# Kernel optimization log

Hardware: AMD Instinct MI355X
Metric: run time of the kernel (lower is better)

Reference implementation:

```python
import jax, jax.numpy as jnp
import numpy as np

B, NS, NQ = 128, 128, 512
D_IN, D_OUT = 256, 64


def setup_inputs() -> dict:
    key = jax.random.key(0)
    ks = jax.random.split(key, 6)
    return {
        "phi_support": jax.random.normal(ks[0], (B, NS, D_IN), dtype=jnp.float32),
        "y_support": jax.random.normal(ks[1], (B, NS, D_OUT), dtype=jnp.float32),
        "phi_query": jax.random.normal(ks[2], (B, NQ, D_IN), dtype=jnp.float32),
        "y_query": jax.random.normal(ks[3], (B, NQ, D_OUT), dtype=jnp.float32),
        # xavier-uniform-ish params
        "m_prior": jax.random.uniform(ks[4], (D_IN, D_OUT), minval=-1.0, maxval=1.0) * np.sqrt(6.0 / (D_IN + D_OUT)),
        "S_inv_prior_asym": jax.random.uniform(ks[5], (D_IN, D_IN), minval=-1.0, maxval=1.0) * np.sqrt(6.0 / (2 * D_IN)),
        "sig_eps": jnp.array([0.1], dtype=jnp.float32),
    }


def reference(phi_support, y_support, phi_query, y_query, m_prior, S_inv_prior_asym, sig_eps):
    alpha = 1.0
    d_out = m_prior.shape[1]
    # prior precision (symmetric PSD by construction) and natural-param prior mean
    S_inv_prior = alpha * (S_inv_prior_asym @ S_inv_prior_asym.T)          # [D_in, D_in]
    m_prior_nat = S_inv_prior @ m_prior                                     # [D_in, D_out]
    # posterior precision / covariance per task (nobs > 0 branch)
    S_inv = jnp.einsum('bni,bnj->bij', phi_support, phi_support) + S_inv_prior  # [B, D_in, D_in]
    S = jnp.linalg.inv(S_inv)                                               # batched small inverse
    rhs = jnp.einsum('bni,bnk->bik', phi_support, y_support) + m_prior_nat  # [B, D_in, D_out]
    m = S @ rhs                                                             # [B, D_in, D_out]
    # predictive mean and spread
    mu = phi_query @ m                                                      # [B, Q, D_out]
    spread_fac = 1.0 + jnp.einsum('bqi,bij,bqj->bq', phi_query, S, phi_query)  # [B, Q]
    # sig = spread_fac (x) (eye * sig_eps) : diagonal [B, Q, D_out, D_out]
    diag = jnp.eye(d_out, dtype=mu.dtype) * sig_eps                         # [D_out, D_out]
    sig = spread_fac[..., None, None] * diag
    # nll: logdet of diagonal sig + quadratic form with its inverse (diag -> reciprocal)
    logdet = d_out * (jnp.log(spread_fac) + jnp.log(sig_eps))               # [B, Q]
    resid = y_query - mu
    quadf = jnp.sum(resid * resid, axis=-1) / (spread_fac * sig_eps)        # [B, Q]
    nll = logdet.mean() + quadf.mean()
    return mu, sig, nll
```

## Files before the change

kernel.cpp:

```cpp
#include <hip/hip_runtime.h>
#include <math.h>

#define B_T   128
#define NS    128
#define NQ    512
#define DIN   256
#define DOUT  64

#define MU_SIZE  (B_T*NQ*DOUT)
#define SIG_SIZE (B_T*NQ*DOUT*DOUT)
#define NLL_IDX  (MU_SIZE + SIG_SIZE)

__global__ __launch_bounds__(256) void k_prior_sp(const float* __restrict__ A,
                                                  double* __restrict__ Sp,
                                                  double* __restrict__ NLLACC) {
    __shared__ float Ai[16][260];
    __shared__ float Aj[16][260];
    int bi = blockIdx.x;
    int i0 = (bi >> 4) << 4;
    int j0 = (bi & 15) << 4;
    int tid = threadIdx.x;
    if (bi == 0 && tid == 0) NLLACC[0] = 0.0;
    for (int idx = tid; idx < 16 * 256; idx += 256) {
        int r = idx >> 8, c = idx & 255;
        Ai[r][c] = A[(i0 + r) * 256 + c];
        Aj[r][c] = A[(j0 + r) * 256 + c];
    }
    __syncthreads();
    int r = tid >> 4, c = tid & 15;
    double acc = 0.0;
    for (int k = 0; k < 256; ++k)
        acc += (double)Ai[r][k] * (double)Aj[c][k];
    Sp[(i0 + r) * 256 + (j0 + c)] = acc;
}

__global__ __launch_bounds__(64) void k_prior_mpn(const double* __restrict__ Sp,
                                                  const float* __restrict__ MP,
                                                  double* __restrict__ MPN) {
    int i = blockIdx.x, k = threadIdx.x;
    double acc = 0.0;
    for (int t = 0; t < 256; ++t)
        acc += Sp[i * 256 + t] * (double)MP[t * 64 + k];
    MPN[i * 64 + k] = acc;
}

__global__ __launch_bounds__(256) void k_build_G(const float* __restrict__ PHI,
                                                 const double* __restrict__ Sp,
                                                 double* __restrict__ G) {
    __shared__ float As[128][64];
    __shared__ float Bs[128][64];
    int b = blockIdx.x;
    int by = blockIdx.y;
    int ti = 0;
    while (((ti + 1) * (ti + 2)) / 2 <= by) ti++;
    int tj = by - (ti * (ti + 1)) / 2;
    int i0 = ti * 64, j0 = tj * 64;
    int tid = threadIdx.x;
    const float* Pb = PHI + b * (NS * DIN);
    for (int idx = tid; idx < 128 * 64; idx += 256) {
        int n = idx >> 6, c = idx & 63;
        As[n][c] = Pb[n * 256 + i0 + c];
        Bs[n][c] = Pb[n * 256 + j0 + c];
    }
    __syncthreads();
    int tx = tid & 15, ty = tid >> 4;
    double acc[4][4];
#pragma unroll
    for (int r = 0; r < 4; ++r)
#pragma unroll
        for (int s = 0; s < 4; ++s) acc[r][s] = 0.0;
    for (int n = 0; n < 128; ++n) {
        float a0 = As[n][4 * ty + 0], a1 = As[n][4 * ty + 1];
        float a2 = As[n][4 * ty + 2], a3 = As[n][4 * ty + 3];
        float b0 = Bs[n][4 * tx + 0], b1 = Bs[n][4 * tx + 1];
        float b2 = Bs[n][4 * tx + 2], b3 = Bs[n][4 * tx + 3];
        acc[0][0] += (double)a0 * b0; acc[0][1] += (double)a0 * b1;
        acc[0][2] += (double)a0 * b2; acc[0][3] += (double)a0 * b3;
        acc[1][0] += (double)a1 * b0; acc[1][1] += (double)a1 * b1;
        acc[1][2] += (double)a1 * b2; acc[1][3] += (double)a1 * b3;
        acc[2][0] += (double)a2 * b0; acc[2][1] += (double)a2 * b1;
        acc[2][2] += (double)a2 * b2; acc[2][3] += (double)a2 * b3;
        acc[3][0] += (double)a3 * b0; acc[3][1] += (double)a3 * b1;
        acc[3][2] += (double)a3 * b2; acc[3][3] += (double)a3 * b3;
    }
    double* Gb = G + b * 65536;
#pragma unroll
    for (int r = 0; r < 4; ++r) {
        int i = i0 + 4 * ty + r;
#pragma unroll
        for (int s = 0; s < 4; ++s) {
            int j = j0 + 4 * tx + s;
            Gb[i * 256 + j] = acc[r][s] + Sp[i * 256 + j];
        }
    }
}

__global__ __launch_bounds__(256) void k_build_rhs(const float* __restrict__ PHI,
                                                   const float* __restrict__ Y,
                                                   const double* __restrict__ MPN,
                                                   double* __restrict__ RHS) {
    __shared__ float As[128][64];
    __shared__ float Ys[128][64];
    int b = blockIdx.x, i0 = blockIdx.y * 64, tid = threadIdx.x;
    const float* Pb = PHI + b * (NS * DIN);
    const float* Yb = Y + b * (NS * DOUT);
    for (int idx = tid; idx < 128 * 64; idx += 256) {
        int n = idx >> 6, c = idx & 63;
        As[n][c] = Pb[n * 256 + i0 + c];
        Ys[n][c] = Yb[n * 64 + c];
    }
    __syncthreads();
    int tx = tid & 15, ty = tid >> 4;
    double acc[4][4];
#pragma unroll
    for (int r = 0; r < 4; ++r)
#pragma unroll
        for (int s = 0; s < 4; ++s) acc[r][s] = 0.0;
    for (int n = 0; n < 128; ++n) {
        float a0 = As[n][4 * ty + 0], a1 = As[n][4 * ty + 1];
        float a2 = As[n][4 * ty + 2], a3 = As[n][4 * ty + 3];
        float y0 = Ys[n][4 * tx + 0], y1 = Ys[n][4 * tx + 1];
        float y2 = Ys[n][4 * tx + 2], y3 = Ys[n][4 * tx + 3];
        acc[0][0] += (double)a0 * y0; acc[0][1] += (double)a0 * y1;
        acc[0][2] += (double)a0 * y2; acc[0][3] += (double)a0 * y3;
        acc[1][0] += (double)a1 * y0; acc[1][1] += (double)a1 * y1;
        acc[1][2] += (double)a1 * y2; acc[1][3] += (double)a1 * y3;
        acc[2][0] += (double)a2 * y0; acc[2][1] += (double)a2 * y1;
        acc[2][2] += (double)a2 * y2; acc[2][3] += (double)a2 * y3;
        acc[3][0] += (double)a3 * y0; acc[3][1] += (double)a3 * y1;
        acc[3][2] += (double)a3 * y2; acc[3][3] += (double)a3 * y3;
    }
    double* Rb = RHS + b * 16384;
#pragma unroll
    for (int r = 0; r < 4; ++r) {
        int i = i0 + 4 * ty + r;
#pragma unroll
        for (int s = 0; s < 4; ++s) {
            int kc = 4 * tx + s;
            Rb[i * 64 + kc] = acc[r][s] + MPN[i * 64 + kc];
        }
    }
}

__global__ __launch_bounds__(256) void k_cholinv(double* __restrict__ G,
                                                 double* __restrict__ LT,
                                                 double* __restrict__ TI,
                                                 float* __restrict__ TIF) {
    __shared__ double S[8192];
    int b = blockIdx.x, tid = threadIdx.x;
    double* Gb = G + b * 65536;
    double* LTb = LT + b * 65536;
    double* TIb = TI + b * 65536;
    float* TIFb = TIF + b * 65536;

    double* P = S;
#define PCH(p, r) P[(p) * 258 + (r)]
    for (int k0 = 0; k0 < 256; k0 += 16) {
        int rows = 256 - k0;
        for (int idx = tid; idx < rows * 16; idx += 256) {
            int r = k0 + (idx >> 4), p = idx & 15;
            PCH(p, r) = Gb[r * 256 + k0 + p];
        }
        __syncthreads();
        for (int p = 0; p < 16; ++p) {
            int k = k0 + p;
            if (tid >= k) {
                double v = PCH(p, tid);
                for (int p2 = 0; p2 < p; ++p2) v -= PCH(p2, tid) * PCH(p2, k);
                PCH(p, tid) = v;
            }
            __syncthreads();
            double d = sqrt(fmax(PCH(p, k), 1e-300));
            double inv = 1.0 / d;
            if (tid > k) PCH(p, tid) *= inv;
            else if (tid == k) PCH(p, tid) = d;
            __syncthreads();
        }
        for (int p = 0; p < 16; ++p) {
            int k = k0 + p;
            if (tid >= k) LTb[k * 256 + tid] = PCH(p, tid);
        }
        int ty = tid >> 4, tx = tid & 15;
        for (int i2 = k0 + 16 + 2 * ty; i2 < 256; i2 += 32) {
            double pa[16], pb[16];
#pragma unroll
            for (int p = 0; p < 16; ++p) { pa[p] = PCH(p, i2); pb[p] = PCH(p, i2 + 1); }
            for (int j2 = k0 + 16 + 2 * tx; j2 <= i2 + 1; j2 += 32) {
                double g00 = 0.0, g01 = 0.0, g10 = 0.0, g11 = 0.0;
#pragma unroll
                for (int p = 0; p < 16; ++p) {
                    double q0 = PCH(p, j2), q1 = PCH(p, j2 + 1);
                    g00 += pa[p] * q0; g01 += pa[p] * q1;
                    g10 += pb[p] * q0; g11 += pb[p] * q1;
                }
                if (j2 <= i2)     Gb[i2 * 256 + j2]           -= g00;
                if (j2 + 1 <= i2) Gb[i2 * 256 + j2 + 1]       -= g01;
                Gb[(i2 + 1) * 256 + j2] -= g10;
                if (j2 <= i2)     Gb[(i2 + 1) * 256 + j2 + 1] -= g11;
            }
        }
        __syncthreads();
    }
#undef PCH

    double* SHD = S;
    for (int idx = tid; idx < 65536; idx += 256) {
        int i = idx >> 8, k = idx & 255;
        if (k > i) { TIb[idx] = 0.0; TIFb[idx] = 0.0f; }
    }
    for (int idx = tid; idx < 8192; idx += 256) {
        int g = idx >> 10, rem = idx & 1023, k = rem >> 5, i = rem & 31;
        SHD[idx] = LTb[(32 * g + k) * 256 + 32 * g + i];
    }
    __syncthreads();
    {
        int g = tid >> 5, j = tid & 31;
        const double* D = SHD + g * 1024;
        double x[32];
#pragma unroll
        for (int i = 0; i < 32; ++i) {
            double s = (i == j) ? 1.0 : 0.0;
#pragma unroll
            for (int k = 0; k < i; ++k) {
                double lv = D[k * 32 + i];
                s -= (k >= j) ? lv * x[k] : 0.0;
            }
            double inv = 1.0 / D[i * 32 + i];
            x[i] = (i >= j) ? s * inv : 0.0;
        }
#pragma unroll
        for (int i = 0; i < 32; ++i) {
            int gi = 32 * g + i, gj = 32 * g + j;
            TIb[gi * 256 + gj] = x[i];
            TIFb[gi * 256 + gj] = (float)x[i];
        }
    }
    __syncthreads();
    double* Bsh = SHD;
    int j = tid & 31, ig = tid >> 5;
    for (int I = 1; I < 8; ++I) {
        for (int J = I - 1; J >= 0; --J) {
            double acc[4] = {0.0, 0.0, 0.0, 0.0};
            for (int K = J; K < I; ++K) {
                for (int kk = 0; kk < 32; ++kk) {
                    double tv = TIb[(32 * K + kk) * 256 + 32 * J + j];
#pragma unroll
                    for (int r = 0; r < 4; ++r) {
                        double lv = LTb[(32 * K + kk) * 256 + 32 * I + ig * 4 + r];
                        acc[r] += lv * tv;
                    }
                }
            }
            __syncthreads();
#pragma unroll
            for (int r = 0; r < 4; ++r) Bsh[(ig * 4 + r) * 32 + j] = acc[r];
            __syncthreads();
            double c[4] = {0.0, 0.0, 0.0, 0.0};
            for (int k = 0; k < 32; ++k) {
                double bv = Bsh[k * 32 + j];
#pragma unroll
                for (int r = 0; r < 4; ++r) {
                    double dv = TIb[(32 * I + ig * 4 + r) * 256 + 32 * I + k];
                    c[r] -= dv * bv;
                }
            }
#pragma unroll
            for (int r = 0; r < 4; ++r) {
                int gi = 32 * I + ig * 4 + r, gj = 32 * J + j;
                TIb[gi * 256 + gj] = c[r];
                TIFb[gi * 256 + gj] = (float)c[r];
            }
        }
        __syncthreads();
    }
}

__global__ __launch_bounds__(256) void k_gemm_Z(const double* __restrict__ TI,
                                                const double* __restrict__ RHS,
                                                double* __restrict__ Z) {
    __shared__ double As[32][64];
    __shared__ double Bs[64][64];
    int b = blockIdx.x, i0 = blockIdx.y * 32;
    int tid = threadIdx.x, c = tid & 63, rg = tid >> 6;
    const double* TIb = TI + b * 65536;
    const double* Rb = RHS + b * 16384;
    double* Zb = Z + b * 16384;
    double acc[8] = {};
    for (int k0 = 0; k0 <= i0; k0 += 64) {
        for (int idx = tid; idx < 2048; idx += 256) {
            int r = idx >> 6, kk = idx & 63;
            As[r][kk] = TIb[(i0 + r) * 256 + k0 + kk];
        }
        for (int idx = tid; idx < 4096; idx += 256) {
            int kk = idx >> 6, cc = idx & 63;
            Bs[kk][cc] = Rb[(k0 + kk) * 64 + cc];
        }
        __syncthreads();
        for (int kk = 0; kk < 64; ++kk) {
            double bv = Bs[kk][c];
#pragma unroll
            for (int r = 0; r < 8; ++r)
                acc[r] += As[rg * 8 + r][kk] * bv;
        }
        __syncthreads();
    }
#pragma unroll
    for (int r = 0; r < 8; ++r)
        Zb[(i0 + rg * 8 + r) * 64 + c] = acc[r];
}

__global__ __launch_bounds__(256) void k_gemm_M(const double* __restrict__ TI,
                                                const double* __restrict__ Z,
                                                double* __restrict__ M) {
    __shared__ double As[64][32];
    __shared__ double Bs[64][64];
    int b = blockIdx.x, i0 = blockIdx.y * 32;
    int tid = threadIdx.x, c = tid & 63, rg = tid >> 6;
    const double* TIb = TI + b * 65536;
    const double* Zb = Z + b * 16384;
    double* Mb = M + b * 16384;
    double acc[8] = {};
    for (int k0 = (i0 >> 6) << 6; k0 < 256; k0 += 64) {
        for (int idx = tid; idx < 2048; idx += 256) {
            int kk = idx >> 5, ri = idx & 31;
            As[kk][ri] = TIb[(k0 + kk) * 256 + i0 + ri];
        }
        for (int idx = tid; idx < 4096; idx += 256) {
            int kk = idx >> 6, cc = idx & 63;
            Bs[kk][cc] = Zb[(k0 + kk) * 64 + cc];
        }
        __syncthreads();
        for (int kk = 0; kk < 64; ++kk) {
            double bv = Bs[kk][c];
#pragma unroll
            for (int r = 0; r < 8; ++r)
                acc[r] += As[kk][rg * 8 + r] * bv;
        }
        __syncthreads();
    }
#pragma unroll
    for (int r = 0; r < 8; ++r)
        Mb[(i0 + rg * 8 + r) * 64 + c] = acc[r];
}

__global__ __launch_bounds__(256) void k_spread_gemm(const float* __restrict__ PHIQ,
                                                     const float* __restrict__ TIF,
                                                     float* __restrict__ PSUM) {
    __shared__ float Qs[64][65];
    __shared__ float Ts[64][65];
    int b = blockIdx.x, q0 = blockIdx.y * 64, I = blockIdx.z, i0 = I * 64;
    int tid = threadIdx.x, tx = tid & 15, ty = tid >> 4;
    const float* Qb = PHIQ + b * (NQ * DIN) + q0 * DIN;
    const float* Tb = TIF + b * 65536;
    float acc[4][4];
#pragma unroll
    for (int r = 0; r < 4; ++r)
#pragma unroll
        for (int s = 0; s < 4; ++s) acc[r][s] = 0.0f;
    for (int k0 = 0; k0 <= i0; k0 += 64) {
        for (int idx = tid; idx < 4096; idx += 256) {
            int r = idx >> 6, c = idx & 63;
            Qs[r][c] = Qb[r * 256 + k0 + c];
            Ts[c][r] = Tb[(i0 + r) * 256 + k0 + c];
        }
        __syncthreads();
        for (int kk = 0; kk < 64; ++kk) {
            float a0 = Qs[4 * ty + 0][kk], a1 = Qs[4 * ty + 1][kk];
            float a2 = Qs[4 * ty + 2][kk], a3 = Qs[4 * ty + 3][kk];
            float b0 = Ts[kk][4 * tx + 0], b1 = Ts[kk][4 * tx + 1];
            float b2 = Ts[kk][4 * tx + 2], b3 = Ts[kk][4 * tx + 3];
            acc[0][0] += a0 * b0; acc[0][1] += a0 * b1; acc[0][2] += a0 * b2; acc[0][3] += a0 * b3;
            acc[1][0] += a1 * b0; acc[1][1] += a1 * b1; acc[1][2] += a1 * b2; acc[1][3] += a1 * b3;
            acc[2][0] += a2 * b0; acc[2][1] += a2 * b1; acc[2][2] += a2 * b2; acc[2][3] += a2 * b3;
            acc[3][0] += a3 * b0; acc[3][1] += a3 * b1; acc[3][2] += a3 * b2; acc[3][3] += a3 * b3;
        }
        __syncthreads();
    }
#pragma unroll
    for (int r = 0; r < 4; ++r) {
        float p = acc[r][0] * acc[r][0] + acc[r][1] * acc[r][1]
                + acc[r][2] * acc[r][2] + acc[r][3] * acc[r][3];
        p += __shfl_down(p, 8, 16);
        p += __shfl_down(p, 4, 16);
        p += __shfl_down(p, 2, 16);
        p += __shfl_down(p, 1, 16);
        if (tx == 0) PSUM[(size_t)(b * 4 + I) * 512 + q0 + 4 * ty + r] = p;
    }
}

__global__ __launch_bounds__(256) void k_mu_nll(const float* __restrict__ PHIQ,
                                                const double* __restrict__ M,
                                                const float* __restrict__ YQ,
                                                const float* __restrict__ PSUM,
                                                const float* __restrict__ SE,
                                                float* __restrict__ SPREAD,
                                                double* __restrict__ NLLACC,
                                                float* __restrict__ MU) {
    __shared__ float Qs[64][65];
    __shared__ float Ms[64][64];
    __shared__ double nred[64];
    int b = blockIdx.x, q0 = blockIdx.y * 64, tid = threadIdx.x;
    int tx = tid & 15, ty = tid >> 4;
    const float* Qb = PHIQ + b * (NQ * DIN) + q0 * DIN;
    const double* Mb = M + b * 16384;
    float acc[4][4];
#pragma unroll
    for (int r = 0; r < 4; ++r)
#pragma unroll
        for (int s = 0; s < 4; ++s) acc[r][s] = 0.0f;
    for (int c0 = 0; c0 < 256; c0 += 64) {
        for (int idx = tid; idx < 4096; idx += 256) {
            int r = idx >> 6, c = idx & 63;
            Qs[r][c] = Qb[r * 256 + c0 + c];
            Ms[r][c] = (float)Mb[(c0 + r) * 64 + c];
        }
        __syncthreads();
        for (int kk = 0; kk < 64; ++kk) {
            float a0 = Qs[4 * ty + 0][kk], a1 = Qs[4 * ty + 1][kk];
            float a2 = Qs[4 * ty + 2][kk], a3 = Qs[4 * ty + 3][kk];
            float b0 = Ms[kk][4 * tx + 0], b1 = Ms[kk][4 * tx + 1];
            float b2 = Ms[kk][4 * tx + 2], b3 = Ms[kk][4 * tx + 3];
            acc[0][0] += a0 * b0; acc[0][1] += a0 * b1; acc[0][2] += a0 * b2; acc[0][3] += a0 * b3;
            acc[1][0] += a1 * b0; acc[1][1] += a1 * b1; acc[1][2] += a1 * b2; acc[1][3] += a1 * b3;
            acc[2][0] += a2 * b0; acc[2][1] += a2 * b1; acc[2][2] += a2 * b2; acc[2][3] += a2 * b3;
            acc[3][0] += a3 * b0; acc[3][1] += a3 * b1; acc[3][2] += a3 * b2; acc[3][3] += a3 * b3;
        }
        __syncthreads();
    }
    float se = SE[0];
#pragma unroll
    for (int r = 0; r < 4; ++r) {
        int q = q0 + 4 * ty + r;
        float4 v = make_float4(acc[r][0], acc[r][1], acc[r][2], acc[r][3]);
        *(float4*)&MU[(b * NQ + q) * 64 + 4 * tx] = v;
        float4 y = *(const float4*)&YQ[(size_t)(b * NQ + q) * 64 + 4 * tx];
        float dx = y.x - v.x, dy = y.y - v.y, dz = y.z - v.z, dw = y.w - v.w;
        float qs = dx * dx + dy * dy + dz * dz + dw * dw;
        qs += __shfl_down(qs, 8, 16);
        qs += __shfl_down(qs, 4, 16);
        qs += __shfl_down(qs, 2, 16);
        qs += __shfl_down(qs, 1, 16);
        if (tx == 0) {
            float sp = 1.0f + PSUM[(size_t)(b * 4 + 0) * 512 + q]
                            + PSUM[(size_t)(b * 4 + 1) * 512 + q]
                            + PSUM[(size_t)(b * 4 + 2) * 512 + q]
                            + PSUM[(size_t)(b * 4 + 3) * 512 + q];
            SPREAD[b * 512 + q] = sp;
            float val = 64.0f * (logf(sp) + logf(se)) + qs / (sp * se);
            nred[ty * 4 + r] = (double)val;
        }
    }
    __syncthreads();
    for (int s = 32; s > 0; s >>= 1) {
        if (tid < s) nred[tid] += nred[tid + s];
        __syncthreads();
    }
    if (tid == 0) atomicAdd(NLLACC, nred[0] * (1.0 / 65536.0));
}

__global__ void k_nll_final(const double* __restrict__ NLLACC,
                            float* __restrict__ out) {
    if (threadIdx.x == 0) out[NLL_IDX] = (float)NLLACC[0];
}

__global__ __launch_bounds__(256) void k_sig(const float* __restrict__ SPREAD,
                                             const float* __restrict__ SE,
                                             float* __restrict__ out) {
    __shared__ float sv_s;
    int bq = blockIdx.x, tid = threadIdx.x;
    if (tid == 0) sv_s = SPREAD[bq] * SE[0];
    __syncthreads();
    float sv = sv_s;
    float* base = out + (size_t)MU_SIZE + (size_t)bq * 4096;
    int i = tid >> 2;
    int jb = (tid & 3) << 4;
    int d = i - jb;
    float vals[16];
#pragma unroll
    for (int t = 0; t < 16; ++t) vals[t] = (t == d) ? sv : 0.0f;
    float4* p = (float4*)(base + tid * 16);
    p[0] = make_float4(vals[0], vals[1], vals[2], vals[3]);
    p[1] = make_float4(vals[4], vals[5], vals[6], vals[7]);
    p[2] = make_float4(vals[8], vals[9], vals[10], vals[11]);
    p[3] = make_float4(vals[12], vals[13], vals[14], vals[15]);
}

extern "C" void kernel_launch(void* const* d_in, const int* in_sizes, int n_in,
                              void* d_out, int out_size, void* d_ws, size_t ws_size,
                              hipStream_t stream) {
    const float* PHI_S = (const float*)d_in[0];
    const float* Y_S   = (const float*)d_in[1];
    const float* PHI_Q = (const float*)d_in[2];
    const float* Y_Q   = (const float*)d_in[3];
    const float* MP    = (const float*)d_in[4];
    const float* AP    = (const float*)d_in[5];
    const float* SE    = (const float*)d_in[6];
    float* out = (float*)d_out;

    double* scratch = (double*)(out + MU_SIZE);
    double* G    = scratch;
    double* LT   = G + 8388608;
    double* RHS  = LT + 8388608;
    double* Z    = RHS + 2097152;
    double* TI   = Z + 2097152;
    double* Spd  = TI + 8388608;
    double* MPN  = Spd + 65536;
    float*  TIF  = (float*)(MPN + 16384);
    float*  PSUM = TIF + 8388608;
    float*  SPREAD = (float*)d_ws;
    double* NLLACC = (double*)((char*)d_ws + 65536 * 4);

    k_prior_sp   <<<256, 256, 0, stream>>>(AP, Spd, NLLACC);
    k_prior_mpn  <<<256, 64, 0, stream>>>(Spd, MP, MPN);
    k_build_G    <<<dim3(B_T, 10), 256, 0, stream>>>(PHI_S, Spd, G);
    k_build_rhs  <<<dim3(B_T, 4), 256, 0, stream>>>(PHI_S, Y_S, MPN, RHS);
    k_cholinv    <<<B_T, 256, 0, stream>>>(G, LT, TI, TIF);
    k_gemm_Z     <<<dim3(B_T, 8), 256, 0, stream>>>(TI, RHS, Z);
    k_gemm_M     <<<dim3(B_T, 8), 256, 0, stream>>>(TI, Z, RHS);
    k_spread_gemm<<<dim3(B_T, 8, 4), 256, 0, stream>>>(PHI_Q, TIF, PSUM);
    k_mu_nll     <<<dim3(B_T, 8), 256, 0, stream>>>(PHI_Q, RHS, Y_Q, PSUM, SE,
                                                    SPREAD, NLLACC, out);
    k_nll_final  <<<1, 64, 0, stream>>>(NLLACC, out);
    k_sig        <<<65536, 256, 0, stream>>>(SPREAD, SE, out);
}
```

Baseline: 2.244 ms.

## Fuse build, solve and predict kernels; widen Cholesky panels to 32 with 512 threads

Merges the prior-mean, G and RHS construction into one launch, and merges the spread GEMM and the mu/NLL computation into one predict kernel that keeps the spread partials in registers. The Cholesky inverse now uses 32-wide panels with a rotated shared layout, shuffle-based panel factorization and 512 threads, and stages the block inverse updates through shared memory. The two M GEMMs are merged into a single solve kernel, and NLL finalization moves into k_sig. This cuts launches and global round-trips, at the cost of more register pressure and more serial work inside the 32-lane panel factorization.

```diff
diff --git a/kernel.cpp b/kernel.cpp
--- a/kernel.cpp
+++ b/kernel.cpp
@@ -34,164 +34,173 @@
     Sp[(i0 + r) * 256 + (j0 + c)] = acc;
 }
 
-__global__ __launch_bounds__(64) void k_prior_mpn(const double* __restrict__ Sp,
-                                                  const float* __restrict__ MP,
-                                                  double* __restrict__ MPN) {
-    int i = blockIdx.x, k = threadIdx.x;
-    double acc = 0.0;
-    for (int t = 0; t < 256; ++t)
-        acc += Sp[i * 256 + t] * (double)MP[t * 64 + k];
-    MPN[i * 64 + k] = acc;
-}
-
-__global__ __launch_bounds__(256) void k_build_G(const float* __restrict__ PHI,
-                                                 const double* __restrict__ Sp,
-                                                 double* __restrict__ G) {
+__global__ __launch_bounds__(256) void k_build(const float* __restrict__ PHI,
+                                               const float* __restrict__ Y,
+                                               const float* __restrict__ MP,
+                                               const double* __restrict__ Sp,
+                                               double* __restrict__ G,
+                                               double* __restrict__ RHS,
+                                               double* __restrict__ MPNo) {
+    int b = blockIdx.x, by = blockIdx.y, tid = threadIdx.x;
+    if (by == 14) {
+        if (b >= 4) return;
+        for (int out = tid; out < 4096; out += 256) {
+            int r = 64 * b + (out >> 6), cc = out & 63;
+            double acc = 0.0;
+            for (int t = 0; t < 256; ++t)
+                acc += Sp[r * 256 + t] * (double)MP[t * 64 + cc];
+            MPNo[r * 64 + cc] = acc;
+        }
+        return;
+    }
     __shared__ float As[128][64];
     __shared__ float Bs[128][64];
-    int b = blockIdx.x;
-    int by = blockIdx.y;
-    int ti = 0;
-    while (((ti + 1) * (ti + 2)) / 2 <= by) ti++;
-    int tj = by - (ti * (ti + 1)) / 2;
-    int i0 = ti * 64, j0 = tj * 64;
-    int tid = threadIdx.x;
+    int tx = tid & 15, ty = tid >> 4;
     const float* Pb = PHI + b * (NS * DIN);
-    for (int idx = tid; idx < 128 * 64; idx += 256) {
-        int n = idx >> 6, c = idx & 63;
-        As[n][c] = Pb[n * 256 + i0 + c];
-        Bs[n][c] = Pb[n * 256 + j0 + c];
-    }
-    __syncthreads();
-    int tx = tid & 15, ty = tid >> 4;
     double acc[4][4];
 #pragma unroll
     for (int r = 0; r < 4; ++r)
 #pragma unroll
         for (int s = 0; s < 4; ++s) acc[r][s] = 0.0;
-    for (int n = 0; n < 128; ++n) {
-        float a0 = As[n][4 * ty + 0], a1 = As[n][4 * ty + 1];
-        float a2 = As[n][4 * ty + 2], a3 = As[n][4 * ty + 3];
-        float b0 = Bs[n][4 * tx + 0], b1 = Bs[n][4 * tx + 1];
-        float b2 = Bs[n][4 * tx + 2], b3 = Bs[n][4 * tx + 3];
-        acc[0][0] += (double)a0 * b0; acc[0][1] += (double)a0 * b1;
-        acc[0][2] += (double)a0 * b2; acc[0][3] += (double)a0 * b3;
-        acc[1][0] += (double)a1 * b0; acc[1][1] += (double)a1 * b1;
-        acc[1][2] += (double)a1 * b2; acc[1][3] += (double)a1 * b3;
-        acc[2][0] += (double)a2 * b0; acc[2][1] += (double)a2 * b1;
-        acc[2][2] += (double)a2 * b2; acc[2][3] += (double)a2 * b3;
-        acc[3][0] += (double)a3 * b0; acc[3][1] += (double)a3 * b1;
-        acc[3][2] += (double)a3 * b2; acc[3][3] += (double)a3 * b3;
-    }
-    double* Gb = G + b * 65536;
-#pragma unroll
-    for (int r = 0; r < 4; ++r) {
-        int i = i0 + 4 * ty + r;
-#pragma unroll
-        for (int s = 0; s < 4; ++s) {
-            int j = j0 + 4 * tx + s;
-            Gb[i * 256 + j] = acc[r][s] + Sp[i * 256 + j];
-        }
-    }
-}
-
-__global__ __launch_bounds__(256) void k_build_rhs(const float* __restrict__ PHI,
-                                                   const float* __restrict__ Y,
-                                                   const double* __restrict__ MPN,
-                                                   double* __restrict__ RHS) {
-    __shared__ float As[128][64];
-    __shared__ float Ys[128][64];
-    int b = blockIdx.x, i0 = blockIdx.y * 64, tid = threadIdx.x;
-    const float* Pb = PHI + b * (NS * DIN);
-    const float* Yb = Y + b * (NS * DOUT);
-    for (int idx = tid; idx < 128 * 64; idx += 256) {
-        int n = idx >> 6, c = idx & 63;
-        As[n][c] = Pb[n * 256 + i0 + c];
-        Ys[n][c] = Yb[n * 64 + c];
-    }
-    __syncthreads();
-    int tx = tid & 15, ty = tid >> 4;
-    double acc[4][4];
-#pragma unroll
-    for (int r = 0; r < 4; ++r)
-#pragma unroll
-        for (int s = 0; s < 4; ++s) acc[r][s] = 0.0;
-    for (int n = 0; n < 128; ++n) {
-        float a0 = As[n][4 * ty + 0], a1 = As[n][4 * ty + 1];
-        float a2 = As[n][4 * ty + 2], a3 = As[n][4 * ty + 3];
-        float y0 = Ys[n][4 * tx + 0], y1 = Ys[n][4 * tx + 1];
-        float y2 = Ys[n][4 * tx + 2], y3 = Ys[n][4 * tx + 3];
-        acc[0][0] += (double)a0 * y0; acc[0][1] += (double)a0 * y1;
-        acc[0][2] += (double)a0 * y2; acc[0][3] += (double)a0 * y3;
-        acc[1][0] += (double)a1 * y0; acc[1][1] += (double)a1 * y1;
-        acc[1][2] += (double)a1 * y2; acc[1][3] += (double)a1 * y3;
-        acc[2][0] += (double)a2 * y0; acc[2][1] += (double)a2 * y1;
-        acc[2][2] += (double)a2 * y2; acc[2][3] += (double)a2 * y3;
-        acc[3][0] += (double)a3 * y0; acc[3][1] += (double)a3 * y1;
-        acc[3][2] += (double)a3 * y2; acc[3][3] += (double)a3 * y3;
-    }
-    double* Rb = RHS + b * 16384;
-#pragma unroll
-    for (int r = 0; r < 4; ++r) {
-        int i = i0 + 4 * ty + r;
-#pragma unroll
-        for (int s = 0; s < 4; ++s) {
-            int kc = 4 * tx + s;
-            Rb[i * 64 + kc] = acc[r][s] + MPN[i * 64 + kc];
-        }
-    }
-}
-
-__global__ __launch_bounds__(256) void k_cholinv(double* __restrict__ G,
+
+    if (by < 10) {
+        int ti = 0;
+        while (((ti + 1) * (ti + 2)) / 2 <= by) ti++;
+        int tj = by - (ti * (ti + 1)) / 2;
+        int i0 = ti * 64, j0 = tj * 64;
+        for (int idx = tid; idx < 128 * 64; idx += 256) {
+            int n = idx >> 6, c = idx & 63;
+            As[n][c] = Pb[n * 256 + i0 + c];
+            Bs[n][c] = Pb[n * 256 + j0 + c];
+        }
+        __syncthreads();
+        for (int n = 0; n < 128; ++n) {
+            float a0 = As[n][4 * ty + 0], a1 = As[n][4 * ty + 1];
+            float a2 = As[n][4 * ty + 2], a3 = As[n][4 * ty + 3];
+            float b0 = Bs[n][4 * tx + 0], b1 = Bs[n][4 * tx + 1];
+            float b2 = Bs[n][4 * tx + 2], b3 = Bs[n][4 * tx + 3];
+            acc[0][0] += (double)a0 * b0; acc[0][1] += (double)a0 * b1;
+            acc[0][2] += (double)a0 * b2; acc[0][3] += (double)a0 * b3;
+            acc[1][0] += (double)a1 * b0; acc[1][1] += (double)a1 * b1;
+            acc[1][2] += (double)a1 * b2; acc[1][3] += (double)a1 * b3;
+            acc[2][0] += (double)a2 * b0; acc[2][1] += (double)a2 * b1;
+            acc[2][2] += (double)a2 * b2; acc[2][3] += (double)a2 * b3;
+            acc[3][0] += (double)a3 * b0; acc[3][1] += (double)a3 * b1;
+            acc[3][2] += (double)a3 * b2; acc[3][3] += (double)a3 * b3;
+        }
+        double* Gb = G + b * 65536;
+#pragma unroll
+        for (int r = 0; r < 4; ++r) {
+            int i = i0 + 4 * ty + r;
+#pragma unroll
+            for (int s = 0; s < 4; ++s) {
+                int j = j0 + 4 * tx + s;
+                Gb[i * 256 + j] = acc[r][s] + Sp[i * 256 + j];
+            }
+        }
+    } else {
+        int i0 = (by - 10) * 64;
+        const float* Yb = Y + b * (NS * DOUT);
+        for (int idx = tid; idx < 128 * 64; idx += 256) {
+            int n = idx >> 6, c = idx & 63;
+            As[n][c] = Pb[n * 256 + i0 + c];
+            Bs[n][c] = Yb[n * 64 + c];
+        }
+        __syncthreads();
+        for (int n = 0; n < 128; ++n) {
+            float a0 = As[n][4 * ty + 0], a1 = As[n][4 * ty + 1];
+            float a2 = As[n][4 * ty + 2], a3 = As[n][4 * ty + 3];
+            float y0 = Bs[n][4 * tx + 0], y1 = Bs[n][4 * tx + 1];
+            float y2 = Bs[n][4 * tx + 2], y3 = Bs[n][4 * tx + 3];
+            acc[0][0] += (double)a0 * y0; acc[0][1] += (double)a0 * y1;
+            acc[0][2] += (double)a0 * y2; acc[0][3] += (double)a0 * y3;
+            acc[1][0] += (double)a1 * y0; acc[1][1] += (double)a1 * y1;
+            acc[1][2] += (double)a1 * y2; acc[1][3] += (double)a1 * y3;
+            acc[2][0] += (double)a2 * y0; acc[2][1] += (double)a2 * y1;
+            acc[2][2] += (double)a2 * y2; acc[2][3] += (double)a2 * y3;
+            acc[3][0] += (double)a3 * y0; acc[3][1] += (double)a3 * y1;
+            acc[3][2] += (double)a3 * y2; acc[3][3] += (double)a3 * y3;
+        }
+        double* Rb = RHS + b * 16384;
+#pragma unroll
+        for (int r = 0; r < 4; ++r) {
+            int i = i0 + 4 * ty + r;
+#pragma unroll
+            for (int s = 0; s < 4; ++s)
+                Rb[i * 64 + 4 * tx + s] = acc[r][s];
+        }
+    }
+}
+
+__global__ __launch_bounds__(512) void k_cholinv(double* __restrict__ G,
                                                  double* __restrict__ LT,
                                                  double* __restrict__ TI,
                                                  float* __restrict__ TIF) {
     __shared__ double S[8192];
+    __shared__ double dinvs[32];
     int b = blockIdx.x, tid = threadIdx.x;
     double* Gb = G + b * 65536;
     double* LTb = LT + b * 65536;
     double* TIb = TI + b * 65536;
     float* TIFb = TIF + b * 65536;
 
-    double* P = S;
-#define PCH(p, r) P[(p) * 258 + (r)]
-    for (int k0 = 0; k0 < 256; k0 += 16) {
+#define PP(p, row) S[(p) * 256 + (((row) + (p)) & 255)]
+    for (int k0 = 0; k0 < 256; k0 += 32) {
         int rows = 256 - k0;
-        for (int idx = tid; idx < rows * 16; idx += 256) {
-            int r = k0 + (idx >> 4), p = idx & 15;
-            PCH(p, r) = Gb[r * 256 + k0 + p];
-        }
-        __syncthreads();
-        for (int p = 0; p < 16; ++p) {
-            int k = k0 + p;
-            if (tid >= k) {
-                double v = PCH(p, tid);
-                for (int p2 = 0; p2 < p; ++p2) v -= PCH(p2, tid) * PCH(p2, k);
-                PCH(p, tid) = v;
-            }
-            __syncthreads();
-            double d = sqrt(fmax(PCH(p, k), 1e-300));
-            double inv = 1.0 / d;
-            if (tid > k) PCH(p, tid) *= inv;
-            else if (tid == k) PCH(p, tid) = d;
-            __syncthreads();
-        }
-        for (int p = 0; p < 16; ++p) {
-            int k = k0 + p;
-            if (tid >= k) LTb[k * 256 + tid] = PCH(p, tid);
+        for (int idx = tid; idx < rows * 32; idx += 512) {
+            int r = k0 + (idx >> 5), p = idx & 31;
+            PP(p, r) = Gb[r * 256 + k0 + p];
+        }
+        __syncthreads();
+        if (tid < 32) {
+            double x[32];
+#pragma unroll
+            for (int p = 0; p < 32; ++p) x[p] = PP(p, k0 + tid);
+            for (int p = 0; p < 32; ++p) {
+                double dpp = __shfl(x[p], p);
+                double d = sqrt(fmax(dpp, 1e-300));
+                double inv = 1.0 / d;
+                if (tid == p) { x[p] = d; dinvs[p] = inv; }
+                else if (tid > p) x[p] *= inv;
+                for (int p2 = p + 1; p2 < 32; ++p2) {
+                    double lp2 = __shfl(x[p], p2);
+                    if (tid >= p2) x[p2] -= x[p] * lp2;
+                }
+            }
+#pragma unroll
+            for (int p = 0; p < 32; ++p) PP(p, k0 + tid) = x[p];
+        }
+        __syncthreads();
+        {
+            int i = k0 + 32 + tid;
+            if (i < 256) {
+                double xr[32];
+#pragma unroll
+                for (int p = 0; p < 32; ++p) {
+                    double v = PP(p, i);
+                    for (int p2 = 0; p2 < p; ++p2)
+                        v -= xr[p2] * PP(p2, k0 + p);
+                    xr[p] = v * dinvs[p];
+                }
+#pragma unroll
+                for (int p = 0; p < 32; ++p) PP(p, i) = xr[p];
+            }
+        }
+        __syncthreads();
+        for (int idx = tid; idx < 8192; idx += 512) {
+            int p = idx >> 8, r = idx & 255;
+            if (r >= k0 + p) LTb[(k0 + p) * 256 + r] = PP(p, r);
         }
         int ty = tid >> 4, tx = tid & 15;
-        for (int i2 = k0 + 16 + 2 * ty; i2 < 256; i2 += 32) {
-            double pa[16], pb[16];
-#pragma unroll
-            for (int p = 0; p < 16; ++p) { pa[p] = PCH(p, i2); pb[p] = PCH(p, i2 + 1); }
-            for (int j2 = k0 + 16 + 2 * tx; j2 <= i2 + 1; j2 += 32) {
+        for (int i2 = k0 + 32 + 2 * ty; i2 < 256; i2 += 64) {
+            for (int j2 = k0 + 32 + 2 * tx; j2 <= i2 + 1; j2 += 32) {
                 double g00 = 0.0, g01 = 0.0, g10 = 0.0, g11 = 0.0;
-#pragma unroll
-                for (int p = 0; p < 16; ++p) {
-                    double q0 = PCH(p, j2), q1 = PCH(p, j2 + 1);
-                    g00 += pa[p] * q0; g01 += pa[p] * q1;
-                    g10 += pb[p] * q0; g11 += pb[p] * q1;
+#pragma unroll 8
+                for (int p = 0; p < 32; ++p) {
+                    double l0 = PP(p, i2), l1 = PP(p, i2 + 1);
+                    double q0 = PP(p, j2), q1 = PP(p, j2 + 1);
+                    g00 += l0 * q0; g01 += l0 * q1;
+                    g10 += l1 * q0; g11 += l1 * q1;
                 }
                 if (j2 <= i2)     Gb[i2 * 256 + j2]           -= g00;
                 if (j2 + 1 <= i2) Gb[i2 * 256 + j2 + 1]       -= g01;
@@ -201,21 +210,20 @@
         }
         __syncthreads();
     }
-#undef PCH
-
-    double* SHD = S;
-    for (int idx = tid; idx < 65536; idx += 256) {
+#undef PP
+
+    for (int idx = tid; idx < 65536; idx += 512) {
         int i = idx >> 8, k = idx & 255;
         if (k > i) { TIb[idx] = 0.0; TIFb[idx] = 0.0f; }
     }
-    for (int idx = tid; idx < 8192; idx += 256) {
+    for (int idx = tid; idx < 8192; idx += 512) {
         int g = idx >> 10, rem = idx & 1023, k = rem >> 5, i = rem & 31;
-        SHD[idx] = LTb[(32 * g + k) * 256 + 32 * g + i];
+        S[idx] = LTb[(32 * g + k) * 256 + 32 * g + i];
     }
     __syncthreads();
-    {
+    if (tid < 256) {
         int g = tid >> 5, j = tid & 31;
-        const double* D = SHD + g * 1024;
+        const double* D = S + g * 1024;
         double x[32];
 #pragma unroll
         for (int i = 0; i < 32; ++i) {
@@ -225,8 +233,7 @@
                 double lv = D[k * 32 + i];
                 s -= (k >= j) ? lv * x[k] : 0.0;
             }
-            double inv = 1.0 / D[i * 32 + i];
-            x[i] = (i >= j) ? s * inv : 0.0;
+            x[i] = (i >= j) ? s * (1.0 / D[i * 32 + i]) : 0.0;
         }
 #pragma unroll
         for (int i = 0; i < 32; ++i) {
@@ -236,183 +243,153 @@
         }
     }
     __syncthreads();
-    double* Bsh = SHD;
-    int j = tid & 31, ig = tid >> 5;
+    double* Lsh = S;
+    double* Tsh = S + 1024;
+    double* Bsh = S + 2048;
+    double* Dsh = S + 3072;
+    int e0 = tid, e1 = tid + 512;
+    int i0e = e0 >> 5, j0e = e0 & 31;
+    int i1e = e1 >> 5, j1e = e1 & 31;
     for (int I = 1; I < 8; ++I) {
+        for (int idx = tid; idx < 1024; idx += 512) {
+            int ii = idx >> 5, kk = idx & 31;
+            Dsh[idx] = TIb[(32 * I + ii) * 256 + 32 * I + kk];
+        }
+        __syncthreads();
         for (int J = I - 1; J >= 0; --J) {
-            double acc[4] = {0.0, 0.0, 0.0, 0.0};
+            double a0 = 0.0, a1 = 0.0;
             for (int K = J; K < I; ++K) {
+                __syncthreads();
+                for (int idx = tid; idx < 1024; idx += 512) {
+                    int kk = idx >> 5, ee = idx & 31;
+                    Lsh[idx] = LTb[(32 * K + kk) * 256 + 32 * I + ee];
+                    Tsh[idx] = TIb[(32 * K + kk) * 256 + 32 * J + ee];
+                }
+                __syncthreads();
+#pragma unroll 8
                 for (int kk = 0; kk < 32; ++kk) {
-                    double tv = TIb[(32 * K + kk) * 256 + 32 * J + j];
-#pragma unroll
-                    for (int r = 0; r < 4; ++r) {
-                        double lv = LTb[(32 * K + kk) * 256 + 32 * I + ig * 4 + r];
-                        acc[r] += lv * tv;
-                    }
-                }
-            }
-            __syncthreads();
-#pragma unroll
-            for (int r = 0; r < 4; ++r) Bsh[(ig * 4 + r) * 32 + j] = acc[r];
-            __syncthreads();
-            double c[4] = {0.0, 0.0, 0.0, 0.0};
-            for (int k = 0; k < 32; ++k) {
-                double bv = Bsh[k * 32 + j];
-#pragma unroll
-                for (int r = 0; r < 4; ++r) {
-                    double dv = TIb[(32 * I + ig * 4 + r) * 256 + 32 * I + k];
-                    c[r] -= dv * bv;
-                }
-            }
-#pragma unroll
-            for (int r = 0; r < 4; ++r) {
-                int gi = 32 * I + ig * 4 + r, gj = 32 * J + j;
-                TIb[gi * 256 + gj] = c[r];
-                TIFb[gi * 256 + gj] = (float)c[r];
-            }
-        }
-        __syncthreads();
-    }
-}
-
-__global__ __launch_bounds__(256) void k_gemm_Z(const double* __restrict__ TI,
-                                                const double* __restrict__ RHS,
-                                                double* __restrict__ Z) {
-    __shared__ double As[32][64];
+                    a0 += Lsh[kk * 32 + i0e] * Tsh[kk * 32 + j0e];
+                    a1 += Lsh[kk * 32 + i1e] * Tsh[kk * 32 + j1e];
+                }
+            }
+            __syncthreads();
+            Bsh[e0] = a0; Bsh[e1] = a1;
+            __syncthreads();
+            double c0 = 0.0, c1 = 0.0;
+#pragma unroll 8
+            for (int kk = 0; kk < 32; ++kk) {
+                c0 -= Dsh[i0e * 32 + kk] * Bsh[kk * 32 + j0e];
+                c1 -= Dsh[i1e * 32 + kk] * Bsh[kk * 32 + j1e];
+            }
+            TIb[(32 * I + i0e) * 256 + 32 * J + j0e] = c0;
+            TIb[(32 * I + i1e) * 256 + 32 * J + j1e] = c1;
+            TIFb[(32 * I + i0e) * 256 + 32 * J + j0e] = (float)c0;
+            TIFb[(32 * I + i1e) * 256 + 32 * J + j1e] = (float)c1;
+            __syncthreads();
+        }
+    }
+}
+
+__global__ __launch_bounds__(512) void k_solve(const double* __restrict__ TI,
+                                               const double* __restrict__ MPN,
+                                               double* __restrict__ RHS,
+                                               double* __restrict__ Z) {
+    __shared__ double As[2048];
     __shared__ double Bs[64][64];
-    int b = blockIdx.x, i0 = blockIdx.y * 32;
-    int tid = threadIdx.x, c = tid & 63, rg = tid >> 6;
+    int b = blockIdx.x, tid = threadIdx.x;
+    int c = tid & 63, rg = tid >> 6;
     const double* TIb = TI + b * 65536;
-    const double* Rb = RHS + b * 16384;
+    double* Rb = RHS + b * 16384;
     double* Zb = Z + b * 16384;
-    double acc[8] = {};
-    for (int k0 = 0; k0 <= i0; k0 += 64) {
-        for (int idx = tid; idx < 2048; idx += 256) {
-            int r = idx >> 6, kk = idx & 63;
-            As[r][kk] = TIb[(i0 + r) * 256 + k0 + kk];
-        }
-        for (int idx = tid; idx < 4096; idx += 256) {
-            int kk = idx >> 6, cc = idx & 63;
-            Bs[kk][cc] = Rb[(k0 + kk) * 64 + cc];
-        }
-        __syncthreads();
-        for (int kk = 0; kk < 64; ++kk) {
-            double bv = Bs[kk][c];
-#pragma unroll
-            for (int r = 0; r < 8; ++r)
-                acc[r] += As[rg * 8 + r][kk] * bv;
-        }
-        __syncthreads();
-    }
-#pragma unroll
-    for (int r = 0; r < 8; ++r)
-        Zb[(i0 + rg * 8 + r) * 64 + c] = acc[r];
-}
-
-__global__ __launch_bounds__(256) void k_gemm_M(const double* __restrict__ TI,
-                                                const double* __restrict__ Z,
-                                                double* __restrict__ M) {
-    __shared__ double As[64][32];
-    __shared__ double Bs[64][64];
-    int b = blockIdx.x, i0 = blockIdx.y * 32;
-    int tid = threadIdx.x, c = tid & 63, rg = tid >> 6;
-    const double* TIb = TI + b * 65536;
-    const double* Zb = Z + b * 16384;
-    double* Mb = M + b * 16384;
-    double acc[8] = {};
-    for (int k0 = (i0 >> 6) << 6; k0 < 256; k0 += 64) {
-        for (int idx = tid; idx < 2048; idx += 256) {
-            int kk = idx >> 5, ri = idx & 31;
-            As[kk][ri] = TIb[(k0 + kk) * 256 + i0 + ri];
-        }
-        for (int idx = tid; idx < 4096; idx += 256) {
-            int kk = idx >> 6, cc = idx & 63;
-            Bs[kk][cc] = Zb[(k0 + kk) * 64 + cc];
-        }
-        __syncthreads();
-        for (int kk = 0; kk < 64; ++kk) {
-            double bv = Bs[kk][c];
-#pragma unroll
-            for (int r = 0; r < 8; ++r)
-                acc[r] += As[kk][rg * 8 + r] * bv;
-        }
-        __syncthreads();
-    }
-#pragma unroll
-    for (int r = 0; r < 8; ++r)
-        Mb[(i0 + rg * 8 + r) * 64 + c] = acc[r];
-}
-
-__global__ __launch_bounds__(256) void k_spread_gemm(const float* __restrict__ PHIQ,
-                                                     const float* __restrict__ TIF,
-                                                     float* __restrict__ PSUM) {
+    for (int i0 = 0; i0 < 8; ++i0) {
+        double acc[4] = {0.0, 0.0, 0.0, 0.0};
+        int ktiles = (i0 >> 1) + 1;
+        for (int kt = 0; kt < ktiles; ++kt) {
+            __syncthreads();
+            for (int idx = tid; idx < 2048; idx += 512) {
+                int rr = idx >> 6, kk = idx & 63;
+                As[rr * 64 + kk] = TIb[(i0 * 32 + rr) * 256 + kt * 64 + kk];
+            }
+            for (int idx = tid; idx < 4096; idx += 512) {
+                int kk = idx >> 6, cc = idx & 63;
+                Bs[kk][cc] = Rb[(kt * 64 + kk) * 64 + cc] + MPN[(kt * 64 + kk) * 64 + cc];
+            }
+            __syncthreads();
+            for (int kk = 0; kk < 64; ++kk) {
+                double bv = Bs[kk][c];
+#pragma unroll
+                for (int u = 0; u < 4; ++u)
+                    acc[u] += As[(rg * 4 + u) * 64 + kk] * bv;
+            }
+        }
+#pragma unroll
+        for (int u = 0; u < 4; ++u)
+            Zb[(i0 * 32 + rg * 4 + u) * 64 + c] = acc[u];
+    }
+    __syncthreads();
+    for (int i0 = 0; i0 < 8; ++i0) {
+        double acc[4] = {0.0, 0.0, 0.0, 0.0};
+        for (int kt = i0 >> 1; kt < 4; ++kt) {
+            __syncthreads();
+            for (int idx = tid; idx < 2048; idx += 512) {
+                int kk = idx >> 5, ri = idx & 31;
+                As[kk * 32 + ri] = TIb[(kt * 64 + kk) * 256 + i0 * 32 + ri];
+            }
+            for (int idx = tid; idx < 4096; idx += 512) {
+                int kk = idx >> 6, cc = idx & 63;
+                Bs[kk][cc] = Zb[(kt * 64 + kk) * 64 + cc];
+            }
+            __syncthreads();
+            for (int kk = 0; kk < 64; ++kk) {
+                double bv = Bs[kk][c];
+#pragma unroll
+                for (int u = 0; u < 4; ++u)
+                    acc[u] += As[kk * 32 + rg * 4 + u] * bv;
+            }
+        }
+#pragma unroll
+        for (int u = 0; u < 4; ++u)
+            Rb[(i0 * 32 + rg * 4 + u) * 64 + c] = acc[u];
+    }
+}
+
+__global__ __launch_bounds__(256) void k_predict(const float* __restrict__ PHIQ,
+                                                 const double* __restrict__ M,
+                                                 const float* __restrict__ TIF,
+                                                 const float* __restrict__ YQ,
+                                                 const float* __restrict__ SE,
+                                                 float* __restrict__ SPREAD,
+                                                 double* __restrict__ NLLACC,
+                                                 float* __restrict__ MU) {
     __shared__ float Qs[64][65];
     __shared__ float Ts[64][65];
-    int b = blockIdx.x, q0 = blockIdx.y * 64, I = blockIdx.z, i0 = I * 64;
-    int tid = threadIdx.x, tx = tid & 15, ty = tid >> 4;
-    const float* Qb = PHIQ + b * (NQ * DIN) + q0 * DIN;
-    const float* Tb = TIF + b * 65536;
-    float acc[4][4];
-#pragma unroll
-    for (int r = 0; r < 4; ++r)
-#pragma unroll
-        for (int s = 0; s < 4; ++s) acc[r][s] = 0.0f;
-    for (int k0 = 0; k0 <= i0; k0 += 64) {
-        for (int idx = tid; idx < 4096; idx += 256) {
-            int r = idx >> 6, c = idx & 63;
-            Qs[r][c] = Qb[r * 256 + k0 + c];
-            Ts[c][r] = Tb[(i0 + r) * 256 + k0 + c];
-        }
-        __syncthreads();
-        for (int kk = 0; kk < 64; ++kk) {
-            float a0 = Qs[4 * ty + 0][kk], a1 = Qs[4 * ty + 1][kk];
-            float a2 = Qs[4 * ty + 2][kk], a3 = Qs[4 * ty + 3][kk];
-            float b0 = Ts[kk][4 * tx + 0], b1 = Ts[kk][4 * tx + 1];
-            float b2 = Ts[kk][4 * tx + 2], b3 = Ts[kk][4 * tx + 3];
-            acc[0][0] += a0 * b0; acc[0][1] += a0 * b1; acc[0][2] += a0 * b2; acc[0][3] += a0 * b3;
-            acc[1][0] += a1 * b0; acc[1][1] += a1 * b1; acc[1][2] += a1 * b2; acc[1][3] += a1 * b3;
-            acc[2][0] += a2 * b0; acc[2][1] += a2 * b1; acc[2][2] += a2 * b2; acc[2][3] += a2 * b3;
-            acc[3][0] += a3 * b0; acc[3][1] += a3 * b1; acc[3][2] += a3 * b2; acc[3][3] += a3 * b3;
-        }
-        __syncthreads();
-    }
-#pragma unroll
-    for (int r = 0; r < 4; ++r) {
-        float p = acc[r][0] * acc[r][0] + acc[r][1] * acc[r][1]
-                + acc[r][2] * acc[r][2] + acc[r][3] * acc[r][3];
-        p += __shfl_down(p, 8, 16);
-        p += __shfl_down(p, 4, 16);
-        p += __shfl_down(p, 2, 16);
-        p += __shfl_down(p, 1, 16);
-        if (tx == 0) PSUM[(size_t)(b * 4 + I) * 512 + q0 + 4 * ty + r] = p;
-    }
-}
-
-__global__ __launch_bounds__(256) void k_mu_nll(const float* __restrict__ PHIQ,
-                                                const double* __restrict__ M,
-                                                const float* __restrict__ YQ,
-                                                const float* __restrict__ PSUM,
-                                                const float* __restrict__ SE,
-                                                float* __restrict__ SPREAD,
-                                                double* __restrict__ NLLACC,
-                                                float* __restrict__ MU) {
-    __shared__ float Qs[64][65];
     __shared__ float Ms[64][64];
     __shared__ double nred[64];
     int b = blockIdx.x, q0 = blockIdx.y * 64, tid = threadIdx.x;
     int tx = tid & 15, ty = tid >> 4;
     const float* Qb = PHIQ + b * (NQ * DIN) + q0 * DIN;
     const double* Mb = M + b * 16384;
-    float acc[4][4];
+    const float* Tb = TIF + b * 65536;
+    float accW[4][4][4];
+    float accM[4][4];
+#pragma unroll
+    for (int I = 0; I < 4; ++I)
+#pragma unroll
+        for (int r = 0; r < 4; ++r)
+#pragma unroll
+            for (int s = 0; s < 4; ++s) accW[I][r][s] = 0.0f;
 #pragma unroll
     for (int r = 0; r < 4; ++r)
 #pragma unroll
-        for (int s = 0; s < 4; ++s) acc[r][s] = 0.0f;
-    for (int c0 = 0; c0 < 256; c0 += 64) {
+        for (int s = 0; s < 4; ++s) accM[r][s] = 0.0f;
+
+    for (int kt = 0; kt < 4; ++kt) {
+        int k0 = kt * 64;
+        __syncthreads();
         for (int idx = tid; idx < 4096; idx += 256) {
-            int r = idx >> 6, c = idx & 63;
-            Qs[r][c] = Qb[r * 256 + c0 + c];
-            Ms[r][c] = (float)Mb[(c0 + r) * 64 + c];
+            int r = idx >> 6, cc = idx & 63;
+            Qs[r][cc] = Qb[r * 256 + k0 + cc];
+            Ms[r][cc] = (float)Mb[(k0 + r) * 64 + cc];
         }
         __syncthreads();
         for (int kk = 0; kk < 64; ++kk) {
@@ -420,34 +397,59 @@
             float a2 = Qs[4 * ty + 2][kk], a3 = Qs[4 * ty + 3][kk];
             float b0 = Ms[kk][4 * tx + 0], b1 = Ms[kk][4 * tx + 1];
             float b2 = Ms[kk][4 * tx + 2], b3 = Ms[kk][4 * tx + 3];
-            acc[0][0] += a0 * b0; acc[0][1] += a0 * b1; acc[0][2] += a0 * b2; acc[0][3] += a0 * b3;
-            acc[1][0] += a1 * b0; acc[1][1] += a1 * b1; acc[1][2] += a1 * b2; acc[1][3] += a1 * b3;
-            acc[2][0] += a2 * b0; acc[2][1] += a2 * b1; acc[2][2] += a2 * b2; acc[2][3] += a2 * b3;
-            acc[3][0] += a3 * b0; acc[3][1] += a3 * b1; acc[3][2] += a3 * b2; acc[3][3] += a3 * b3;
-        }
-        __syncthreads();
+            accM[0][0] += a0 * b0; accM[0][1] += a0 * b1; accM[0][2] += a0 * b2; accM[0][3] += a0 * b3;
+            accM[1][0] += a1 * b0; accM[1][1] += a1 * b1; accM[1][2] += a1 * b2; accM[1][3] += a1 * b3;
+            accM[2][0] += a2 * b0; accM[2][1] += a2 * b1; accM[2][2] += a2 * b2; accM[2][3] += a2 * b3;
+            accM[3][0] += a3 * b0; accM[3][1] += a3 * b1; accM[3][2] += a3 * b2; accM[3][3] += a3 * b3;
+        }
+#pragma unroll
+        for (int I = 0; I < 4; ++I) {
+            if (I >= kt) {
+                __syncthreads();
+                for (int idx = tid; idx < 4096; idx += 256) {
+                    int r = idx >> 6, cc = idx & 63;
+                    Ts[cc][r] = Tb[(I * 64 + r) * 256 + k0 + cc];
+                }
+                __syncthreads();
+                for (int kk = 0; kk < 64; ++kk) {
+                    float a0 = Qs[4 * ty + 0][kk], a1 = Qs[4 * ty + 1][kk];
+                    float a2 = Qs[4 * ty + 2][kk], a3 = Qs[4 * ty + 3][kk];
+                    float b0 = Ts[kk][4 * tx + 0], b1 = Ts[kk][4 * tx + 1];
+                    float b2 = Ts[kk][4 * tx + 2], b3 = Ts[kk][4 * tx + 3];
+                    accW[I][0][0] += a0 * b0; accW[I][0][1] += a0 * b1; accW[I][0][2] += a0 * b2; accW[I][0][3] += a0 * b3;
+                    accW[I][1][0] += a1 * b0; accW[I][1][1] += a1 * b1; accW[I][1][2] += a1 * b2; accW[I][1][3] += a1 * b3;
+                    accW[I][2][0] += a2 * b0; accW[I][2][1] += a2 * b1; accW[I][2][2] += a2 * b2; accW[I][2][3] += a2 * b3;
+                    accW[I][3][0] += a3 * b0; accW[I][3][1] += a3 * b1; accW[I][3][2] += a3 * b2; accW[I][3][3] += a3 * b3;
+                }
+            }
+        }
     }
     float se = SE[0];
 #pragma unroll
     for (int r = 0; r < 4; ++r) {
         int q = q0 + 4 * ty + r;
-        float4 v = make_float4(acc[r][0], acc[r][1], acc[r][2], acc[r][3]);
-        *(float4*)&MU[(b * NQ + q) * 64 + 4 * tx] = v;
-        float4 y = *(const float4*)&YQ[(size_t)(b * NQ + q) * 64 + 4 * tx];
+        float4 v = make_float4(accM[r][0], accM[r][1], accM[r][2], accM[r][3]);
+        *(float4*)&MU[((size_t)b * NQ + q) * 64 + 4 * tx] = v;
+        float4 y = *(const float4*)&YQ[((size_t)b * NQ + q) * 64 + 4 * tx];
         float dx = y.x - v.x, dy = y.y - v.y, dz = y.z - v.z, dw = y.w - v.w;
         float qs = dx * dx + dy * dy + dz * dz + dw * dw;
+        float p = 0.0f;
+#pragma unroll
+        for (int I = 0; I < 4; ++I)
+#pragma unroll
+            for (int s = 0; s < 4; ++s) p += accW[I][r][s] * accW[I][r][s];
         qs += __shfl_down(qs, 8, 16);
         qs += __shfl_down(qs, 4, 16);
         qs += __shfl_down(qs, 2, 16);
         qs += __shfl_down(qs, 1, 16);
+        p += __shfl_down(p, 8, 16);
+        p += __shfl_down(p, 4, 16);
+        p += __shfl_down(p, 2, 16);
+        p += __shfl_down(p, 1, 16);
         if (tx == 0) {
-            float sp = 1.0f + PSUM[(size_t)(b * 4 + 0) * 512 + q]
-                            + PSUM[(size_t)(b * 4 + 1) * 512 + q]
-                            + PSUM[(size_t)(b * 4 + 2) * 512 + q]
-                            + PSUM[(size_t)(b * 4 + 3) * 512 + q];
+            float sp = 1.0f + p;
             SPREAD[b * 512 + q] = sp;
-            float val = 64.0f * (logf(sp) + logf(se)) + qs / (sp * se);
-            nred[ty * 4 + r] = (double)val;
+            nred[ty * 4 + r] = (double)(64.0f * (logf(sp) + logf(se)) + qs / (sp * se));
         }
     }
     __syncthreads();
@@ -458,16 +460,13 @@
     if (tid == 0) atomicAdd(NLLACC, nred[0] * (1.0 / 65536.0));
 }
 
-__global__ void k_nll_final(const double* __restrict__ NLLACC,
-                            float* __restrict__ out) {
-    if (threadIdx.x == 0) out[NLL_IDX] = (float)NLLACC[0];
-}
-
 __global__ __launch_bounds__(256) void k_sig(const float* __restrict__ SPREAD,
                                              const float* __restrict__ SE,
+                                             const double* __restrict__ NLLACC,
                                              float* __restrict__ out) {
     __shared__ float sv_s;
     int bq = blockIdx.x, tid = threadIdx.x;
+    if (bq == 0 && tid == 0) out[NLL_IDX] = (float)NLLACC[0];
     if (tid == 0) sv_s = SPREAD[bq] * SE[0];
     __syncthreads();
     float sv = sv_s;
@@ -506,20 +505,14 @@
     double* Spd  = TI + 8388608;
     double* MPN  = Spd + 65536;
     float*  TIF  = (float*)(MPN + 16384);
-    float*  PSUM = TIF + 8388608;
     float*  SPREAD = (float*)d_ws;
     double* NLLACC = (double*)((char*)d_ws + 65536 * 4);
 
-    k_prior_sp   <<<256, 256, 0, stream>>>(AP, Spd, NLLACC);
-    k_prior_mpn  <<<256, 64, 0, stream>>>(Spd, MP, MPN);
-    k_build_G    <<<dim3(B_T, 10), 256, 0, stream>>>(PHI_S, Spd, G);
-    k_build_rhs  <<<dim3(B_T, 4), 256, 0, stream>>>(PHI_S, Y_S, MPN, RHS);
-    k_cholinv    <<<B_T, 256, 0, stream>>>(G, LT, TI, TIF);
-    k_gemm_Z     <<<dim3(B_T, 8), 256, 0, stream>>>(TI, RHS, Z);
-    k_gemm_M     <<<dim3(B_T, 8), 256, 0, stream>>>(TI, Z, RHS);
-    k_spread_gemm<<<dim3(B_T, 8, 4), 256, 0, stream>>>(PHI_Q, TIF, PSUM);
-    k_mu_nll     <<<dim3(B_T, 8), 256, 0, stream>>>(PHI_Q, RHS, Y_Q, PSUM, SE,
-                                                    SPREAD, NLLACC, out);
-    k_nll_final  <<<1, 64, 0, stream>>>(NLLACC, out);
-    k_sig        <<<65536, 256, 0, stream>>>(SPREAD, SE, out);
-}
+    k_prior_sp<<<256, 256, 0, stream>>>(AP, Spd, NLLACC);
+    k_build   <<<dim3(B_T, 15), 256, 0, stream>>>(PHI_S, Y_S, MP, Spd, G, RHS, MPN);
+    k_cholinv <<<B_T, 512, 0, stream>>>(G, LT, TI, TIF);
+    k_solve   <<<B_T, 512, 0, stream>>>(TI, MPN, RHS, Z);
+    k_predict <<<dim3(B_T, 8), 256, 0, stream>>>(PHI_Q, RHS, TIF, Y_Q, SE,
+                                                 SPREAD, NLLACC, out);
+    k_sig     <<<65536, 256, 0, stream>>>(SPREAD, SE, NLLACC, out);
+}
```

After: 3.320 ms. +47.9%, slower.
